# Optimization experiments

Hardware: AMD Instinct MI355X
Metric: run time of the kernel (lower is better)

## Reference

```python
import jax, jax.numpy as jnp
import numpy as np

SCALE = 15.0
BIG = 1e9  # masked-out distances; exp(-SCALE*BIG) underflows to exactly 0 in fp32
P, M, N, D, NCAM = 6, 512, 4096, 1024, 8
FEAT_STD = 0.03  # keep squared distances O(1) so exp(-scale*d) doesn't underflow


def setup_inputs() -> dict:
    key = jax.random.key(0)
    k1, k2, k3, k4 = jax.random.split(key, 4)
    feature = jax.random.normal(k1, (P, M, D), dtype=jnp.float32) * FEAT_STD
    centers = jax.random.normal(k2, (P, N, D), dtype=jnp.float32) * FEAT_STD
    camid = jax.random.randint(k3, (M,), 0, NCAM)   # camera id per sample
    cam = jax.random.randint(k4, (N,), 0, NCAM)     # camera id per center
    return {"feature": feature, "camid": camid, "centers": centers, "cam": cam}


def _explog(x):
    # faithful to torch: (-scale * x).exp().sum().log(), per row (last axis)
    return jnp.log(jnp.sum(jnp.exp(-SCALE * x), axis=-1))


def reference(feature, camid, centers, cam):
    p, m, d = feature.shape
    n = centers.shape[1]
    # squared euclidean distance map per part: [P, m, n]
    f2 = jnp.sum(feature * feature, axis=-1)            # [P, m]
    c2 = jnp.sum(centers * centers, axis=-1)            # [P, n]
    dist = f2[:, :, None] + c2[:, None, :] - 2.0 * jnp.einsum('pmd,pnd->pmn', feature, centers)
    # intra mask: center cam == sample cam  (same for all parts)
    mask = camid[:, None] == cam[None, :]               # [m, n]
    # push masked-out entries to BIG so ascending sort puts them last and exp(-s*BIG)=0
    d_intra = jnp.sort(jnp.where(mask[None, :, :], dist, BIG), axis=-1)   # [P, m, n]
    d_inter = jnp.sort(jnp.where(mask[None, :, :], BIG, dist), axis=-1)   # [P, m, n]
    x_intra = _explog(d_intra[..., :4])
    y_intra = _explog(d_intra[..., 6:])
    x_inter = _explog(d_inter[..., :8])
    y_inter = _explog(d_inter[..., 12:])
    hinge_intra = jnp.maximum(-x_intra + y_intra + 12.0, 0.0)
    hinge_inter = jnp.maximum(-x_inter + y_inter + 5.0, 0.0)
    loss = jnp.sum(hinge_intra + hinge_inter) / (m * p)
    return loss
```

## Files before the change

### kernel.cpp

```cpp
#include <hip/hip_runtime.h>
#include <math.h>

#define PP 6
#define MM 512
#define NN 4096
#define DD 1024
#define KSCALE 15.0f
#define BIGV 1e9f

#define BM 128
#define BN 128
#define BK 16
#define NCHUNK (DD / BK)
#define NSTRIP (NN / BN)
#define KI 6
#define KR 12
#define PARTW 20
#define LDSB 16384

typedef __bf16 bf16x8 __attribute__((ext_vector_type(8)));
typedef float  f32x16 __attribute__((ext_vector_type(16)));

__device__ __forceinline__ void insert6(float (&a)[KI], float v) {
    if (v < a[KI - 1]) {
        float cur = v;
#pragma unroll
        for (int x = 0; x < KI; ++x) {
            float lo = fminf(a[x], cur);
            float hi = fmaxf(a[x], cur);
            a[x] = lo; cur = hi;
        }
    }
}
__device__ __forceinline__ void insert12(float (&a)[KR], float v) {
    if (v < a[KR - 1]) {
        float cur = v;
#pragma unroll
        for (int x = 0; x < KR; ++x) {
            float lo = fminf(a[x], cur);
            float hi = fmaxf(a[x], cur);
            a[x] = lo; cur = hi;
        }
    }
}


__global__ __launch_bounds__(256)
void decomp_feat(const float* __restrict__ f,
                 __bf16* __restrict__ hi, __bf16* __restrict__ lo) {
    size_t base = ((size_t)blockIdx.x * 256 + threadIdx.x) * 8;
    float4 v0 = *(const float4*)(f + base);
    float4 v1 = *(const float4*)(f + base + 4);
    float fv[8] = {v0.x, v0.y, v0.z, v0.w, v1.x, v1.y, v1.z, v1.w};
    bf16x8 h, l;
#pragma unroll
    for (int i = 0; i < 8; ++i) {
        __bf16 hh = (__bf16)fv[i];
        h[i] = hh;
        l[i] = (__bf16)(fv[i] - (float)hh);
    }
    *(bf16x8*)(hi + base) = h;
    *(bf16x8*)(lo + base) = l;
}

__global__ __launch_bounds__(256)
void decomp_cent(const float* __restrict__ cz,
                 __bf16* __restrict__ hi, __bf16* __restrict__ lo,
                 float* __restrict__ c2, float* __restrict__ out) {
    if (blockIdx.x == 0 && threadIdx.x == 0) out[0] = 0.0f;
    const int row  = blockIdx.x * 4 + (threadIdx.x >> 6);
    const int lane = threadIdx.x & 63;
    const size_t eb = (size_t)row * DD + lane * 16;
    float s = 0.0f;
#pragma unroll
    for (int g = 0; g < 2; ++g) {
        float4 v0 = *(const float4*)(cz + eb + g * 8);
        float4 v1 = *(const float4*)(cz + eb + g * 8 + 4);
        float fv[8] = {v0.x, v0.y, v0.z, v0.w, v1.x, v1.y, v1.z, v1.w};
        bf16x8 h, l;
#pragma unroll
        for (int i = 0; i < 8; ++i) {
            s = fmaf(fv[i], fv[i], s);
            __bf16 hh = (__bf16)fv[i];
            h[i] = hh;
            l[i] = (__bf16)(fv[i] - (float)hh);
        }
        *(bf16x8*)(hi + eb + g * 8) = h;
        *(bf16x8*)(lo + eb + g * 8) = l;
    }
#pragma unroll
    for (int off = 32; off > 0; off >>= 1) s += __shfl_down(s, off, 64);
    if (lane == 0) c2[row] = s;
}


__global__ __launch_bounds__(256, 3)
void dist_topk_kernel(const __bf16* __restrict__ Fhi, const __bf16* __restrict__ Flo,
                      const __bf16* __restrict__ Chi, const __bf16* __restrict__ Clo,
                      const float* __restrict__ c2g,
                      const int* __restrict__ camid, const int* __restrict__ cam,
                      float* __restrict__ partials) {
    const int ns = blockIdx.x;
    const int mt = blockIdx.y;
    const int p  = blockIdx.z;
    const int t  = threadIdx.x;
    const int lane = t & 63, w = t >> 6;
    const int wr = w >> 1, wc = w & 1;
    const int l31 = lane & 31, lh = lane >> 5;

    __shared__ __align__(16) char smem[2 * LDSB + 128 * 33 * 4];
    __shared__ int s_cam[BN];
    float* bandS = (float*)(smem + 2 * LDSB);

    if (t < BN) s_cam[t] = cam[ns * BN + t];

    const char* srcp[4];
    int ldsoff[4];
#pragma unroll
    for (int i = 0; i < 4; ++i) {
        const int r_idx = w * 4 + i;
        const int plane = r_idx >> 3;
        const int ks    = (r_idx >> 2) & 1;
        const int row   = (r_idx & 3) * 64 + lane;
        const __bf16* basep;
        size_t gr;
        if (row < BM) { basep = plane ? Flo : Fhi; gr = (size_t)(p * MM + mt * BM + row) * DD; }
        else          { basep = plane ? Clo : Chi; gr = (size_t)(p * NN + ns * BN + row - BM) * DD; }
        srcp[i]   = (const char*)(basep + gr + ks * 8);
        ldsoff[i] = r_idx * 1024;
    }

    int aU[2], bU[2];
#pragma unroll
    for (int x = 0; x < 2; ++x) {
        aU[x] = (lh * 256 + wr * 64 + x * 32 + l31) * 16;
        bU[x] = (lh * 256 + 128 + wc * 64 + x * 32 + l31) * 16;
    }

    f32x16 acc[2][2];
#pragma unroll
    for (int i = 0; i < 2; ++i)
#pragma unroll
        for (int j = 0; j < 2; ++j)
#pragma unroll
            for (int r = 0; r < 16; ++r) acc[i][j][r] = 0.0f;

    auto stage = [&](int buf, int c) {
#pragma unroll
        for (int i = 0; i < 4; ++i)
            __builtin_amdgcn_global_load_lds(
                (const __attribute__((address_space(1))) void*)(srcp[i] + (size_t)c * 32),
                (__attribute__((address_space(3))) void*)(smem + buf * LDSB + ldsoff[i]),
                16, 0, 0);
    };

    stage(0, 0);
    __syncthreads();

    for (int c = 0; c < NCHUNK; ++c) {
        const int cur = c & 1;
        if (c + 1 < NCHUNK) stage(cur ^ 1, c + 1);
        const char* bb = smem + cur * LDSB;
        bf16x8 ah[2], al[2], bh[2], bl[2];
#pragma unroll
        for (int x = 0; x < 2; ++x) {
            ah[x] = *(const bf16x8*)(bb + aU[x]);
            al[x] = *(const bf16x8*)(bb + 8192 + aU[x]);
            bh[x] = *(const bf16x8*)(bb + bU[x]);
            bl[x] = *(const bf16x8*)(bb + 8192 + bU[x]);
        }
#pragma unroll
        for (int mi = 0; mi < 2; ++mi)
#pragma unroll
            for (int nj = 0; nj < 2; ++nj) {
                acc[mi][nj] = __builtin_amdgcn_mfma_f32_32x32x16_bf16(
                    ah[mi], bh[nj], acc[mi][nj], 0, 0, 0);
                acc[mi][nj] = __builtin_amdgcn_mfma_f32_32x32x16_bf16(
                    ah[mi], bl[nj], acc[mi][nj], 0, 0, 0);
                acc[mi][nj] = __builtin_amdgcn_mfma_f32_32x32x16_bf16(
                    al[mi], bh[nj], acc[mi][nj], 0, 0, 0);
            }
        __syncthreads();
    }

    float c2v[2];
#pragma unroll
    for (int nj = 0; nj < 2; ++nj)
        c2v[nj] = c2g[p * NN + ns * BN + wc * 64 + nj * 32 + l31];

    const int myrow = t >> 1, half = t & 1;
    const int my_cam = camid[mt * BM + myrow];
    float ti[KI], tr[KR];
#pragma unroll
    for (int x = 0; x < KI; ++x) ti[x] = BIGV;
#pragma unroll
    for (int x = 0; x < KR; ++x) tr[x] = BIGV;
    float si = 0.0f, sr = 0.0f;

#pragma unroll
    for (int b = 0; b < 4; ++b) {
        __syncthreads();
        if (wc == (b >> 1)) {
            const int nj = b & 1;
#pragma unroll
            for (int mi = 0; mi < 2; ++mi)
#pragma unroll
                for (int r = 0; r < 16; ++r) {
                    int R = wr * 64 + mi * 32 + (r & 3) + 8 * (r >> 2) + 4 * lh;
                    bandS[R * 33 + l31] = c2v[nj] - 2.0f * acc[mi][nj][r];
                }
        }
        __syncthreads();
        const float* drow = bandS + myrow * 33 + half * 16;
        const int*   crow = s_cam + b * 32 + half * 16;
#pragma unroll
        for (int j = 0; j < 16; ++j) {
            float dd = drow[j];
            float e  = __expf(-KSCALE * dd);
            if (crow[j] == my_cam) { si += e; insert6(ti, dd); }
            else                   { sr += e; insert12(tr, dd); }
        }
    }

    float oti[KI], otr[KR];
#pragma unroll
    for (int x = 0; x < KI; ++x) oti[x] = __shfl_xor(ti[x], 1, 64);
#pragma unroll
    for (int x = 0; x < KR; ++x) otr[x] = __shfl_xor(tr[x], 1, 64);
    float osi = __shfl_xor(si, 1, 64), osr = __shfl_xor(sr, 1, 64);
#pragma unroll
    for (int x = 0; x < KI; ++x) insert6(ti, oti[x]);
#pragma unroll
    for (int x = 0; x < KR; ++x) insert12(tr, otr[x]);
    si += osi; sr += osr;

    if (!half) {
        float* outp = partials +
            ((size_t)(p * MM + mt * BM + myrow) * NSTRIP + ns) * PARTW;
#pragma unroll
        for (int x = 0; x < KI; ++x) outp[x] = ti[x];
#pragma unroll
        for (int x = 0; x < KR; ++x) outp[KI + x] = tr[x];
        outp[18] = si; outp[19] = sr;
    }
}


__global__ __launch_bounds__(256)
void finalize_kernel(const float* __restrict__ partials, float* __restrict__ out) {
    const int t = threadIdx.x, lane = t & 63, w = t >> 6;
    const int row = blockIdx.x * 4 + w;
    const int strip = lane & 31;
    const float* q = partials + ((size_t)row * NSTRIP + strip) * PARTW;
    float ti[KI], tr[KR];
#pragma unroll
    for (int x = 0; x < KI; ++x) ti[x] = q[x];
#pragma unroll
    for (int x = 0; x < KR; ++x) tr[x] = q[KI + x];
    float si = q[18], sr = q[19];

#pragma unroll
    for (int s = 1; s < 32; s <<= 1) {
        float oti[KI], otr[KR];
#pragma unroll
        for (int x = 0; x < KI; ++x) oti[x] = __shfl_xor(ti[x], s, 64);
#pragma unroll
        for (int x = 0; x < KR; ++x) otr[x] = __shfl_xor(tr[x], s, 64);
        float osi = __shfl_xor(si, s, 64), osr = __shfl_xor(sr, s, 64);
#pragma unroll
        for (int x = 0; x < KI; ++x) insert6(ti, oti[x]);
#pragma unroll
        for (int x = 0; x < KR; ++x) insert12(tr, otr[x]);
        si += osi; sr += osr;
    }

    if (lane == 0) {
        float ei[KI], er[KR];
#pragma unroll
        for (int x = 0; x < KI; ++x) ei[x] = __expf(-KSCALE * ti[x]);
#pragma unroll
        for (int x = 0; x < KR; ++x) er[x] = __expf(-KSCALE * tr[x]);
        float x_intra = logf(ei[0] + ei[1] + ei[2] + ei[3]);
        float top6 = ei[0] + ei[1] + ei[2] + ei[3] + ei[4] + ei[5];
        float y_intra = logf(fmaxf(si - top6, 0.0f));
        float x_inter = logf(er[0] + er[1] + er[2] + er[3] +
                             er[4] + er[5] + er[6] + er[7]);
        float top12 = 0.0f;
#pragma unroll
        for (int x = 0; x < KR; ++x) top12 += er[x];
        float y_inter = logf(fmaxf(sr - top12, 0.0f));
        float h = fmaxf(y_intra - x_intra + 12.0f, 0.0f) +
                  fmaxf(y_inter - x_inter + 5.0f, 0.0f);
        atomicAdd(out, h * (1.0f / (MM * PP)));
    }
}

extern "C" void kernel_launch(void* const* d_in, const int* in_sizes, int n_in,
                              void* d_out, int out_size, void* d_ws, size_t ws_size,
                              hipStream_t stream) {
    const float* feature = (const float*)d_in[0];
    const int*   camid   = (const int*)  d_in[1];
    const float* centers = (const float*)d_in[2];
    const int*   cam     = (const int*)  d_in[3];
    float* out = (float*)d_out;

    char* ws = (char*)d_ws;
    __bf16* Chi = (__bf16*)(ws);
    __bf16* Clo = (__bf16*)(ws + 50331648);
    __bf16* Fhi = (__bf16*)(ws + 100663296);
    __bf16* Flo = (__bf16*)(ws + 106954752);
    float*  c2  = (float*) (ws + 113246208);
    float*  partials = (float*)(ws + 113344512);

    decomp_feat<<<(PP * MM * DD / 8) / 256, 256, 0, stream>>>(feature, Fhi, Flo);
    decomp_cent<<<(PP * NN) / 4, 256, 0, stream>>>(centers, Chi, Clo, c2, out);
    dim3 grid(NSTRIP, MM / BM, PP);
    dist_topk_kernel<<<grid, 256, 0, stream>>>(Fhi, Flo, Chi, Clo, c2,
                                               camid, cam, partials);
    finalize_kernel<<<(PP * MM) / 4, 256, 0, stream>>>(partials, out);
}
```

Baseline: 358.3 us.

## Deepen LDS pipeline to four buffers with vmcnt waits and merge decomposition kernels

Replaces the double-buffered global_load_lds loop with a 4-stage ring that prefetches three chunks ahead, waits on vmcnt counts instead of a full sync each iteration, and raises MFMA priority with s_setprio. The epilogue band buffer now aliases the staging LDS, which is sized for four buffers. Occupancy hint drops from 3 to 2 blocks. The two bf16 split kernels are fused into one launch. The deeper prefetch is meant to hide global latency better, at the cost of larger LDS and lower occupancy.

New measurement: 385.4 us. 1.08x slower.

```diff
diff --git a/kernel.cpp b/kernel.cpp
--- a/kernel.cpp
+++ b/kernel.cpp
@@ -17,6 +17,7 @@
 #define KR 12
 #define PARTW 20
 #define LDSB 16384
+#define NBUF 4
 
 typedef __bf16 bf16x8 __attribute__((ext_vector_type(8)));
 typedef float  f32x16 __attribute__((ext_vector_type(16)));
@@ -46,36 +47,25 @@
 
 
 __global__ __launch_bounds__(256)
-void decomp_feat(const float* __restrict__ f,
-                 __bf16* __restrict__ hi, __bf16* __restrict__ lo) {
-    size_t base = ((size_t)blockIdx.x * 256 + threadIdx.x) * 8;
-    float4 v0 = *(const float4*)(f + base);
-    float4 v1 = *(const float4*)(f + base + 4);
-    float fv[8] = {v0.x, v0.y, v0.z, v0.w, v1.x, v1.y, v1.z, v1.w};
-    bf16x8 h, l;
-#pragma unroll
-    for (int i = 0; i < 8; ++i) {
-        __bf16 hh = (__bf16)fv[i];
-        h[i] = hh;
-        l[i] = (__bf16)(fv[i] - (float)hh);
-    }
-    *(bf16x8*)(hi + base) = h;
-    *(bf16x8*)(lo + base) = l;
-}
-
-__global__ __launch_bounds__(256)
-void decomp_cent(const float* __restrict__ cz,
-                 __bf16* __restrict__ hi, __bf16* __restrict__ lo,
-                 float* __restrict__ c2, float* __restrict__ out) {
+void decomp_all(const float* __restrict__ feature, const float* __restrict__ centers,
+                __bf16* __restrict__ Fhi, __bf16* __restrict__ Flo,
+                __bf16* __restrict__ Chi, __bf16* __restrict__ Clo,
+                float* __restrict__ c2, float* __restrict__ out) {
     if (blockIdx.x == 0 && threadIdx.x == 0) out[0] = 0.0f;
-    const int row  = blockIdx.x * 4 + (threadIdx.x >> 6);
+    const int r    = blockIdx.x * 4 + (threadIdx.x >> 6);
     const int lane = threadIdx.x & 63;
+    const float* src;
+    __bf16 *dhi, *dlo;
+    int row;
+    bool isC;
+    if (r < PP * MM) { src = feature; dhi = Fhi; dlo = Flo; row = r; isC = false; }
+    else             { src = centers; dhi = Chi; dlo = Clo; row = r - PP * MM; isC = true; }
     const size_t eb = (size_t)row * DD + lane * 16;
     float s = 0.0f;
 #pragma unroll
     for (int g = 0; g < 2; ++g) {
-        float4 v0 = *(const float4*)(cz + eb + g * 8);
-        float4 v1 = *(const float4*)(cz + eb + g * 8 + 4);
+        float4 v0 = *(const float4*)(src + eb + g * 8);
+        float4 v1 = *(const float4*)(src + eb + g * 8 + 4);
         float fv[8] = {v0.x, v0.y, v0.z, v0.w, v1.x, v1.y, v1.z, v1.w};
         bf16x8 h, l;
 #pragma unroll
@@ -85,16 +75,16 @@
             h[i] = hh;
             l[i] = (__bf16)(fv[i] - (float)hh);
         }
-        *(bf16x8*)(hi + eb + g * 8) = h;
-        *(bf16x8*)(lo + eb + g * 8) = l;
+        *(bf16x8*)(dhi + eb + g * 8) = h;
+        *(bf16x8*)(dlo + eb + g * 8) = l;
     }
 #pragma unroll
     for (int off = 32; off > 0; off >>= 1) s += __shfl_down(s, off, 64);
-    if (lane == 0) c2[row] = s;
-}
-
-
-__global__ __launch_bounds__(256, 3)
+    if (isC && lane == 0) c2[row] = s;
+}
+
+
+__global__ __launch_bounds__(256, 2)
 void dist_topk_kernel(const __bf16* __restrict__ Fhi, const __bf16* __restrict__ Flo,
                       const __bf16* __restrict__ Chi, const __bf16* __restrict__ Clo,
                       const float* __restrict__ c2g,
@@ -108,11 +98,9 @@
     const int wr = w >> 1, wc = w & 1;
     const int l31 = lane & 31, lh = lane >> 5;
 
-    __shared__ __align__(16) char smem[2 * LDSB + 128 * 33 * 4];
+    __shared__ __align__(16) char smem[NBUF * LDSB];
     __shared__ int s_cam[BN];
-    float* bandS = (float*)(smem + 2 * LDSB);
-
-    if (t < BN) s_cam[t] = cam[ns * BN + t];
+    float* bandS = (float*)smem;
 
     const char* srcp[4];
     int ldsoff[4];
@@ -154,13 +142,16 @@
                 16, 0, 0);
     };
 
-    stage(0, 0);
-    __syncthreads();
+    stage(0, 0); stage(1, 1); stage(2, 2);
 
     for (int c = 0; c < NCHUNK; ++c) {
-        const int cur = c & 1;
-        if (c + 1 < NCHUNK) stage(cur ^ 1, c + 1);
-        const char* bb = smem + cur * LDSB;
+        if (c + 2 < NCHUNK)      asm volatile("s_waitcnt vmcnt(8)" ::: "memory");
+        else if (c + 1 < NCHUNK) asm volatile("s_waitcnt vmcnt(4)" ::: "memory");
+        else                     asm volatile("s_waitcnt vmcnt(0)" ::: "memory");
+        __builtin_amdgcn_s_barrier();
+        if (c + 3 < NCHUNK) stage((c + 3) & 3, c + 3);
+
+        const char* bb = smem + (c & 3) * LDSB;
         bf16x8 ah[2], al[2], bh[2], bl[2];
 #pragma unroll
         for (int x = 0; x < 2; ++x) {
@@ -169,6 +160,9 @@
             bh[x] = *(const bf16x8*)(bb + bU[x]);
             bl[x] = *(const bf16x8*)(bb + 8192 + bU[x]);
         }
+        asm volatile("s_waitcnt lgkmcnt(0)" ::: "memory");
+        __builtin_amdgcn_sched_barrier(0);
+        __builtin_amdgcn_s_setprio(1);
 #pragma unroll
         for (int mi = 0; mi < 2; ++mi)
 #pragma unroll
@@ -180,9 +174,12 @@
                 acc[mi][nj] = __builtin_amdgcn_mfma_f32_32x32x16_bf16(
                     al[mi], bh[nj], acc[mi][nj], 0, 0, 0);
             }
-        __syncthreads();
-    }
-
+        __builtin_amdgcn_s_setprio(0);
+    }
+
+    __syncthreads();
+
+    if (t < BN) s_cam[t] = cam[ns * BN + t];
     float c2v[2];
 #pragma unroll
     for (int nj = 0; nj < 2; ++nj)
@@ -312,8 +309,9 @@
     float*  c2  = (float*) (ws + 113246208);
     float*  partials = (float*)(ws + 113344512);
 
-    decomp_feat<<<(PP * MM * DD / 8) / 256, 256, 0, stream>>>(feature, Fhi, Flo);
-    decomp_cent<<<(PP * NN) / 4, 256, 0, stream>>>(centers, Chi, Clo, c2, out);
+    decomp_all<<<(PP * (MM + NN)) / 4, 256, 0, stream>>>(feature, centers,
+                                                         Fhi, Flo, Chi, Clo,
+                                                         c2, out);
     dim3 grid(NSTRIP, MM / BM, PP);
     dist_topk_kernel<<<grid, 256, 0, stream>>>(Fhi, Flo, Chi, Clo, c2,
                                                camid, cam, partials);
```
